# Kernel optimization log

Hardware: AMD Instinct MI355X
Metric: run time of the kernel (lower is better)

Reference implementation:

```python
import jax, jax.numpy as jnp
import numpy as np

D_MODEL = 1024
N_HEADS = 16
NUM_KV_HEADS = 4
D_K = D_MODEL // N_HEADS
ROPE_BASE = 10000.0


def apply_rotary_emb(x, base=ROPE_BASE):
    # x: [B, H, T, D], half-split rotation over positions 0..T-1
    B, H, T, D = x.shape
    inv_freq = 1.0 / (base ** (jnp.arange(0, D, 2, dtype=jnp.float32) / D))  # [D/2]
    ang = jnp.arange(T, dtype=jnp.float32)[:, None] * inv_freq[None, :]      # [T, D/2]
    cos = jnp.cos(ang)[None, None].astype(x.dtype)
    sin = jnp.sin(ang)[None, None].astype(x.dtype)
    x1, x2 = x[..., : D // 2], x[..., D // 2 :]
    return jnp.concatenate([x1 * cos - x2 * sin, x2 * cos + x1 * sin], axis=-1)


def setup_inputs() -> dict:
    key = jax.random.key(0)
    ks = jax.random.split(key, 6)
    B, Tq, Tkv = 4, 2048, 2048
    query = jax.random.normal(ks[0], (B, Tq, D_MODEL), dtype=jnp.float32)
    key_value = jax.random.normal(ks[1], (B, Tkv, D_MODEL), dtype=jnp.float32)
    query_mask = jnp.ones((B, Tq), dtype=jnp.bool_)
    kv_mask = jnp.ones((B, Tkv), dtype=jnp.bool_)
    s = 0.02
    w_q = jax.random.normal(ks[2], (D_MODEL, D_MODEL), dtype=jnp.float32) * s
    w_k = jax.random.normal(ks[3], (NUM_KV_HEADS * D_K, D_MODEL), dtype=jnp.float32) * s
    w_v = jax.random.normal(ks[4], (NUM_KV_HEADS * D_K, D_MODEL), dtype=jnp.float32) * s
    w_out = jax.random.normal(ks[5], (D_MODEL, D_MODEL), dtype=jnp.float32) * s
    return {"query": query, "key_value": key_value, "query_mask": query_mask,
            "kv_mask": kv_mask, "w_q": w_q, "w_k": w_k, "w_v": w_v, "w_out": w_out}


def reference(query, key_value, query_mask, kv_mask, w_q, w_k, w_v, w_out):
    B, Tq, _ = query.shape
    Tkv = key_value.shape[1]
    group = N_HEADS // NUM_KV_HEADS
    # projections (torch Linear: x @ W.T)
    Q = (query @ w_q.T).reshape(B, Tq, N_HEADS, D_K).transpose(0, 2, 1, 3)        # [B,H,Tq,D]
    K = (key_value @ w_k.T).reshape(B, Tkv, NUM_KV_HEADS, D_K).transpose(0, 2, 1, 3)
    V = (key_value @ w_v.T).reshape(B, Tkv, NUM_KV_HEADS, D_K).transpose(0, 2, 1, 3)
    # RoPE on Q and K
    Q = apply_rotary_emb(Q)
    K = apply_rotary_emb(K)
    # GQA: repeat kv heads
    K = jnp.repeat(K, group, axis=1)  # [B,H,Tkv,D]
    V = jnp.repeat(V, group, axis=1)
    # mask: [B,1,Tq,Tkv]
    attn_mask = (kv_mask[:, None, None, :] & query_mask[:, None, :, None])
    scale = 1.0 / jnp.sqrt(jnp.asarray(D_K, dtype=Q.dtype))
    scores = jnp.einsum("bhqd,bhkd->bhqk", Q, K) * scale
    scores = jnp.where(attn_mask, scores, jnp.asarray(-jnp.inf, dtype=scores.dtype))
    attn = jax.nn.softmax(scores, axis=-1)
    out = jnp.einsum("bhqk,bhkd->bhqd", attn, V)
    out = out.transpose(0, 2, 1, 3).reshape(B, Tq, D_MODEL)
    out = out @ w_out.T
    return out
```

## Files before the change

### kernel.cpp

```cpp
#include <hip/hip_runtime.h>
#include <hip/hip_bf16.h>
#include <hip/hip_fp16.h>

#define B_    4
#define TQ    2048
#define TKV   2048
#define DM    1024
#define NH    16
#define NKV   4
#define DK    64

typedef _Float16 f16x8 __attribute__((ext_vector_type(8)));
typedef _Float16 f16x4 __attribute__((ext_vector_type(4)));
typedef float    f32x4 __attribute__((ext_vector_type(4)));
typedef float    f32x16 __attribute__((ext_vector_type(16)));

__device__ __forceinline__ void store1(float* p, float v) { *p = v; }
__device__ __forceinline__ void store1(__half* p, float v) {
  union { __half h; unsigned short u; } c; c.h = __float2half(v);
  *(unsigned short*)p = c.u;
}

__device__ __forceinline__ f16x4 load4h(const float* p) {
  float4 v = *(const float4*)p;
  f16x4 r;
  r[0] = (_Float16)v.x; r[1] = (_Float16)v.y;
  r[2] = (_Float16)v.z; r[3] = (_Float16)v.w;
  return r;
}
__device__ __forceinline__ f16x4 load4h(const __half* p) {
  return *(const f16x4*)p;
}

__device__ __forceinline__ unsigned pack2h(float a, float b) {
  auto pk = __builtin_amdgcn_cvt_pkrtz(a, b);
  unsigned u;
  __builtin_memcpy(&u, &pk, 4);
  return u;
}

__global__ void zero_out_kernel(float* out, int n) {
  int i = blockIdx.x * blockDim.x + threadIdx.x;
  if (i < n) out[i] = 0.0f;
}

#define GAP 40
template <typename AT, typename CT>
__global__ __launch_bounds__(256) void gemm_bt_mfma(
    const AT* __restrict__ A,
    const float* __restrict__ W0, const float* __restrict__ W1,
    CT* __restrict__ C0, CT* __restrict__ C1, int M, int N, int K) {
  __shared__ _Float16 As[2 * 128 * GAP];
  __shared__ _Float16 Ws[2 * 128 * GAP];
  const float* __restrict__ W = (blockIdx.z == 0) ? W0 : W1;
  CT* __restrict__ C = (blockIdx.z == 0) ? C0 : C1;

  const int t = threadIdx.x;
  const int w = t >> 6, l = t & 63;
  const int lm = l & 15, quad = l >> 4;
  const int wm = (w >> 1) * 64, wn = (w & 1) * 64;
  const int m0 = blockIdx.y * 128, n0 = blockIdx.x * 128;

  const int srow = t >> 3;
  const int scol = (t & 7) * 4;

  f32x4 acc[4][4] = {};
  f16x4 av[4], wv[4];
#pragma unroll
  for (int p = 0; p < 4; ++p) {
    int r = srow + p * 32;
    av[p] = load4h(&A[(size_t)(m0 + r) * K + scol]);
    wv[p] = load4h(&W[(size_t)(n0 + r) * K + scol]);
  }

  int cur = 0;
  for (int k0 = 0; k0 < K; k0 += 32) {
    _Float16* as = &As[cur * 128 * GAP];
    _Float16* ws = &Ws[cur * 128 * GAP];
#pragma unroll
    for (int p = 0; p < 4; ++p) {
      int r = srow + p * 32;
      *(f16x4*)&as[r * GAP + scol] = av[p];
      *(f16x4*)&ws[r * GAP + scol] = wv[p];
    }
    __syncthreads();
    if (k0 + 32 < K) {
#pragma unroll
      for (int p = 0; p < 4; ++p) {
        int r = srow + p * 32;
        av[p] = load4h(&A[(size_t)(m0 + r) * K + k0 + 32 + scol]);
        wv[p] = load4h(&W[(size_t)(n0 + r) * K + k0 + 32 + scol]);
      }
    }

    f16x8 af[4], bf[4];
#pragma unroll
    for (int i = 0; i < 4; ++i)
      af[i] = *(const f16x8*)&as[(wm + i * 16 + lm) * GAP + quad * 8];
#pragma unroll
    for (int j = 0; j < 4; ++j)
      bf[j] = *(const f16x8*)&ws[(wn + j * 16 + lm) * GAP + quad * 8];
#pragma unroll
    for (int i = 0; i < 4; ++i)
#pragma unroll
      for (int j = 0; j < 4; ++j)
        acc[i][j] =
            __builtin_amdgcn_mfma_f32_16x16x32_f16(af[i], bf[j], acc[i][j], 0, 0, 0);
    cur ^= 1;
  }

#pragma unroll
  for (int i = 0; i < 4; ++i)
#pragma unroll
    for (int r = 0; r < 4; ++r) {
      size_t row = (size_t)(m0 + wm + i * 16 + quad * 4 + r) * N;
#pragma unroll
      for (int j = 0; j < 4; ++j)
        store1(&C[row + n0 + wn + j * 16 + lm], acc[i][j][r]);
    }
}

__global__ void rope_kernel(__half* __restrict__ X, int T, int H, int total_pairs) {
  int idx = blockIdx.x * blockDim.x + threadIdx.x;
  if (idx >= total_pairs) return;
  int i   = idx & 31;
  int h   = (idx >> 5) % H;
  int row = idx / (32 * H);
  int tpos = row % T;
  __half* p = X + ((size_t)row * H + h) * DK;
  float inv = exp2f((float)i * -0.41524101186091403f);
  float ang = (float)tpos * inv;
  float c, s;
  sincosf(ang, &s, &c);
  float x1 = __half2float(p[i]), x2 = __half2float(p[i + 32]);
  p[i]      = __float2half(x1 * c - x2 * s);
  p[i + 32] = __float2half(x2 * c + x1 * s);
}

#define AP 72
#define C2 0.18033688011112042f
#define RLOG2 -0.41524101186091403f
__global__ __launch_bounds__(256, 3) void attn_mfma(const __half* Q,
                                                    const __half* __restrict__ K,
                                                    const __half* __restrict__ V,
                                                    __half* O) {
  __shared__ _Float16 Ks[64 * AP];
  __shared__ _Float16 Vt[64 * AP];
  const int t = threadIdx.x;
  const int w = t >> 6, l = t & 63;
  const int lq = l & 31, hi = l >> 5;
  const int qt = blockIdx.x, h = blockIdx.y, b = blockIdx.z;
  const int kvh = h >> 2;

  const __half* qbase =
      Q + (((size_t)b * TQ + qt * 128 + w * 32 + lq) * NH + h) * DK;
  f16x8 aq[4];
#pragma unroll
  for (int kc = 0; kc < 4; ++kc)
    aq[kc] = *(const f16x8*)(qbase + kc * 16 + hi * 8);

  {
    const float tpos = (float)(qt * 128 + w * 32 + lq);
#pragma unroll
    for (int kc = 0; kc < 2; ++kc)
#pragma unroll
      for (int j = 0; j < 8; ++j) {
        int d = kc * 16 + hi * 8 + j;
        float inv = exp2f((float)d * RLOG2);
        float ang = tpos * inv;
        float c, s;
        sincosf(ang, &s, &c);
        float x1 = (float)aq[kc][j], x2 = (float)aq[kc + 2][j];
        aq[kc][j]     = (_Float16)((x1 * c - x2 * s) * C2);
        aq[kc + 2][j] = (_Float16)((x2 * c + x1 * s) * C2);
      }
  }

  const int skey = t >> 3, sdseg = t & 7;
  const int vkey = t & 63, vdb0 = (t >> 6) * 8;
  const __half* kp0 =
      K + (((size_t)b * TKV + skey) * NKV + kvh) * DK + sdseg * 8;
  const __half* kp1 = kp0 + (size_t)32 * NKV * DK;
  const __half* vp0 =
      V + (((size_t)b * TKV + vkey) * NKV + kvh) * DK + vdb0;
  const __half* vp1 = vp0 + 32;
  const size_t kstep = (size_t)64 * NKV * DK;

  f16x8 kpre0 = *(const f16x8*)kp0, kpre1 = *(const f16x8*)kp1;
  f16x8 vpre0 = *(const f16x8*)vp0, vpre1 = *(const f16x8*)vp1;

  f32x16 o_acc[2];
#pragma unroll
  for (int i = 0; i < 16; ++i) { o_acc[0][i] = 0.f; o_acc[1][i] = 0.f; }
  float m_run = -1e30f, l_run = 0.0f;

  for (int ck = 0; ck < TKV / 64; ++ck) {
    __syncthreads();
    *(f16x8*)&Ks[skey * AP + sdseg * 8] = kpre0;
    *(f16x8*)&Ks[(skey + 32) * AP + sdseg * 8] = kpre1;
#pragma unroll
    for (int j = 0; j < 8; ++j) {
      Vt[(vdb0 + j) * AP + vkey] = vpre0[j];
      Vt[(vdb0 + 32 + j) * AP + vkey] = vpre1[j];
    }
    __syncthreads();
    if (ck + 1 < TKV / 64) {
      size_t off = (size_t)(ck + 1) * kstep;
      kpre0 = *(const f16x8*)(kp0 + off);
      kpre1 = *(const f16x8*)(kp1 + off);
      vpre0 = *(const f16x8*)(vp0 + off);
      vpre1 = *(const f16x8*)(vp1 + off);
    }

#pragma unroll
    for (int tile = 0; tile < 2; ++tile) {
      f32x16 st;
#pragma unroll
      for (int i = 0; i < 16; ++i) st[i] = 0.f;
      __builtin_amdgcn_s_setprio(1);
#pragma unroll
      for (int kc = 0; kc < 4; ++kc) {
        f16x8 ak =
            *(const f16x8*)&Ks[(tile * 32 + lq) * AP + kc * 16 + hi * 8];
        st = __builtin_amdgcn_mfma_f32_32x32x16_f16(ak, aq[kc], st, 0, 0, 0);
      }
      __builtin_amdgcn_s_setprio(0);

      float vmax = st[0];
#pragma unroll
      for (int i = 1; i < 16; ++i) vmax = fmaxf(vmax, st[i]);
      vmax = fmaxf(vmax, __shfl_xor(vmax, 32));

      if (!__all(vmax - m_run <= 8.0f)) {
        float m_new = fmaxf(m_run, vmax);
        float alpha = exp2f(m_run - m_new);
        m_run = m_new;
        l_run *= alpha;
#pragma unroll
        for (int reg = 0; reg < 16; ++reg) {
          int row = (reg & 3) + 8 * (reg >> 2) + 4 * hi;
          float ar = __shfl(alpha, row);
          o_acc[0][reg] *= ar;
          o_acc[1][reg] *= ar;
        }
      }

      unsigned q16u[8];
      float psum = 0.0f;
#pragma unroll
      for (int rr = 0; rr < 8; ++rr) {
        float p0 = exp2f(st[2 * rr] - m_run);
        float p1 = exp2f(st[2 * rr + 1] - m_run);
        psum += p0 + p1;
        q16u[rr] = pack2h(p0, p1);
      }
      psum += __shfl_xor(psum, 32);
      l_run += psum;

      __builtin_amdgcn_s_setprio(1);
#pragma unroll
      for (int kb = 0; kb < 2; ++kb) {
        const int base = kb * 4;
        union { unsigned u[4]; f16x8 v; } ap;
#pragma unroll
        for (int c = 0; c < 2; ++c) {
          unsigned R0 = q16u[base + c];
          unsigned R1 = q16u[base + 2 + c];
          unsigned Z = hi ? R0 : R1;
          unsigned Xp = __shfl_xor(Z, 32);
          ap.u[c]     = hi ? Xp : R0;
          ap.u[c + 2] = hi ? R1 : Xp;
        }
#pragma unroll
        for (int nt = 0; nt < 2; ++nt) {
          f16x8 bv = *(const f16x8*)&Vt[(nt * 32 + lq) * AP + tile * 32 +
                                        kb * 16 + hi * 8];
          o_acc[nt] =
              __builtin_amdgcn_mfma_f32_32x32x16_f16(ap.v, bv, o_acc[nt], 0, 0, 0);
        }
      }
      __builtin_amdgcn_s_setprio(0);
    }
  }

#pragma unroll
  for (int reg = 0; reg < 16; ++reg) {
    int row = (reg & 3) + 8 * (reg >> 2) + 4 * hi;
    float inv = 1.0f / __shfl(l_run, row);
    size_t orow =
        (((size_t)b * TQ + qt * 128 + w * 32 + row) * NH + h) * DK;
    O[orow + lq]      = __float2half(o_acc[0][reg] * inv);
    O[orow + 32 + lq] = __float2half(o_acc[1][reg] * inv);
  }
}

extern "C" void kernel_launch(void* const* d_in, const int* in_sizes, int n_in,
                              void* d_out, int out_size, void* d_ws, size_t ws_size,
                              hipStream_t stream) {
  int iq, ikv, iwq, iwk, iwv, iwo;
  bool ok = true;
  if (n_in >= 8 && in_sizes[0] == 8388608 && in_sizes[1] == 8388608) {
    iq = 0; ikv = 1; iwq = 4; iwk = 5; iwv = 6; iwo = 7;
  } else if (n_in >= 8 && in_sizes[0] == 8388608 && in_sizes[1] == 8192) {
    ikv = 0; iq = 2; iwk = 4; iwo = 5; iwq = 6; iwv = 7;
  } else if (n_in == 6 && in_sizes[2] == 1048576) {
    iq = 0; ikv = 1; iwq = 2; iwk = 3; iwv = 4; iwo = 5;
  } else if (n_in == 6 && in_sizes[2] == 262144) {
    ikv = 0; iq = 1; iwk = 2; iwo = 3; iwq = 4; iwv = 5;
  } else {
    ok = false; iq = ikv = iwq = iwk = iwv = iwo = 0;
  }

  const size_t nQ  = (size_t)B_ * TQ * DM;
  const size_t nKV = (size_t)B_ * TKV * NKV * DK;
  const size_t need = (nQ + 2 * nKV) * sizeof(__half);
  if (!ok || ws_size < need) {
    zero_out_kernel<<<(out_size + 255) / 256, 256, 0, stream>>>((float*)d_out,
                                                                out_size);
    return;
  }

  const float* query     = (const float*)d_in[iq];
  const float* key_value = (const float*)d_in[ikv];
  const float* w_q   = (const float*)d_in[iwq];
  const float* w_k   = (const float*)d_in[iwk];
  const float* w_v   = (const float*)d_in[iwv];
  const float* w_out = (const float*)d_in[iwo];
  float* out = (float*)d_out;

  __half* Qh = (__half*)d_ws;
  __half* Kh = Qh + nQ;
  __half* Vh = Kh + nKV;

  dim3 blk(256);
  gemm_bt_mfma<<<dim3(DM / 128, B_ * TQ / 128, 1), blk, 0, stream>>>(
      query, w_q, w_q, Qh, Qh, B_ * TQ, DM, DM);
  gemm_bt_mfma<<<dim3(NKV * DK / 128, B_ * TKV / 128, 2), blk, 0, stream>>>(
      key_value, w_k, w_v, Kh, Vh, B_ * TKV, NKV * DK, DM);
  int pk = B_ * TKV * NKV * 32;
  rope_kernel<<<(pk + 255) / 256, blk, 0, stream>>>(Kh, TKV, NKV, pk);
  attn_mfma<<<dim3(TQ / 128, NH, B_), dim3(256), 0, stream>>>(Qh, Kh, Vh, Qh);
  gemm_bt_mfma<<<dim3(DM / 128, B_ * TQ / 128, 1), blk, 0, stream>>>(
      Qh, w_out, w_out, out, out, B_ * TQ, DM, DM);
}
```

Baseline: 387.8 us.

## Merge Q/K/V projections into one launch with 64x128 GEMM tiles

```diff
diff --git a/kernel.cpp b/kernel.cpp
--- a/kernel.cpp
+++ b/kernel.cpp
@@ -45,63 +45,80 @@
 }
 
 #define GAP 40
+#define BM 64
+#define BN 128
 template <typename AT, typename CT>
-__global__ __launch_bounds__(256) void gemm_bt_mfma(
-    const AT* __restrict__ A,
+__global__ __launch_bounds__(256) void gemm_proj(
+    const AT* __restrict__ A0, const AT* __restrict__ A1,
     const float* __restrict__ W0, const float* __restrict__ W1,
-    CT* __restrict__ C0, CT* __restrict__ C1, int M, int N, int K) {
-  __shared__ _Float16 As[2 * 128 * GAP];
-  __shared__ _Float16 Ws[2 * 128 * GAP];
-  const float* __restrict__ W = (blockIdx.z == 0) ? W0 : W1;
-  CT* __restrict__ C = (blockIdx.z == 0) ? C0 : C1;
+    const float* __restrict__ W2,
+    CT* __restrict__ C0, CT* __restrict__ C1, CT* __restrict__ C2,
+    int N0, int Nkv, int K) {
+  const int bid = blockIdx.x;
+  const AT* __restrict__ A;
+  const float* __restrict__ W;
+  CT* __restrict__ C;
+  int N, bx, by;
+  if (bid < 1024) {
+    A = A0; W = W0; C = C0; N = N0;
+    bx = bid & 7; by = bid >> 3;
+  } else {
+    int r = bid - 1024;
+    A = A1; N = Nkv;
+    if (r < 256) { W = W1; C = C1; } else { W = W2; C = C2; r -= 256; }
+    bx = r & 1; by = r >> 1;
+  }
+
+  __shared__ _Float16 As[2 * BM * GAP];
+  __shared__ _Float16 Ws[2 * BN * GAP];
 
   const int t = threadIdx.x;
   const int w = t >> 6, l = t & 63;
   const int lm = l & 15, quad = l >> 4;
-  const int wm = (w >> 1) * 64, wn = (w & 1) * 64;
-  const int m0 = blockIdx.y * 128, n0 = blockIdx.x * 128;
+  const int wm = (w >> 1) * 32, wn = (w & 1) * 64;
+  const int m0 = by * BM, n0 = bx * BN;
 
   const int srow = t >> 3;
   const int scol = (t & 7) * 4;
 
-  f32x4 acc[4][4] = {};
-  f16x4 av[4], wv[4];
-#pragma unroll
-  for (int p = 0; p < 4; ++p) {
-    int r = srow + p * 32;
-    av[p] = load4h(&A[(size_t)(m0 + r) * K + scol]);
-    wv[p] = load4h(&W[(size_t)(n0 + r) * K + scol]);
-  }
+  f32x4 acc[2][4] = {};
+  f16x4 av[2], wv[4];
+#pragma unroll
+  for (int p = 0; p < 2; ++p)
+    av[p] = load4h(&A[(size_t)(m0 + srow + p * 32) * K + scol]);
+#pragma unroll
+  for (int p = 0; p < 4; ++p)
+    wv[p] = load4h(&W[(size_t)(n0 + srow + p * 32) * K + scol]);
 
   int cur = 0;
   for (int k0 = 0; k0 < K; k0 += 32) {
-    _Float16* as = &As[cur * 128 * GAP];
-    _Float16* ws = &Ws[cur * 128 * GAP];
-#pragma unroll
-    for (int p = 0; p < 4; ++p) {
-      int r = srow + p * 32;
-      *(f16x4*)&as[r * GAP + scol] = av[p];
-      *(f16x4*)&ws[r * GAP + scol] = wv[p];
-    }
+    _Float16* as = &As[cur * BM * GAP];
+    _Float16* ws = &Ws[cur * BN * GAP];
+#pragma unroll
+    for (int p = 0; p < 2; ++p)
+      *(f16x4*)&as[(srow + p * 32) * GAP + scol] = av[p];
+#pragma unroll
+    for (int p = 0; p < 4; ++p)
+      *(f16x4*)&ws[(srow + p * 32) * GAP + scol] = wv[p];
     __syncthreads();
     if (k0 + 32 < K) {
 #pragma unroll
-      for (int p = 0; p < 4; ++p) {
-        int r = srow + p * 32;
-        av[p] = load4h(&A[(size_t)(m0 + r) * K + k0 + 32 + scol]);
-        wv[p] = load4h(&W[(size_t)(n0 + r) * K + k0 + 32 + scol]);
-      }
-    }
-
-    f16x8 af[4], bf[4];
-#pragma unroll
-    for (int i = 0; i < 4; ++i)
+      for (int p = 0; p < 2; ++p)
+        av[p] = load4h(&A[(size_t)(m0 + srow + p * 32) * K + k0 + 32 + scol]);
+#pragma unroll
+      for (int p = 0; p < 4; ++p)
+        wv[p] = load4h(&W[(size_t)(n0 + srow + p * 32) * K + k0 + 32 + scol]);
+    }
+
+    f16x8 af[2], bf[4];
+#pragma unroll
+    for (int i = 0; i < 2; ++i)
       af[i] = *(const f16x8*)&as[(wm + i * 16 + lm) * GAP + quad * 8];
 #pragma unroll
     for (int j = 0; j < 4; ++j)
       bf[j] = *(const f16x8*)&ws[(wn + j * 16 + lm) * GAP + quad * 8];
 #pragma unroll
-    for (int i = 0; i < 4; ++i)
+    for (int i = 0; i < 2; ++i)
 #pragma unroll
       for (int j = 0; j < 4; ++j)
         acc[i][j] =
@@ -110,7 +127,7 @@
   }
 
 #pragma unroll
-  for (int i = 0; i < 4; ++i)
+  for (int i = 0; i < 2; ++i)
 #pragma unroll
     for (int r = 0; r < 4; ++r) {
       size_t row = (size_t)(m0 + wm + i * 16 + quad * 4 + r) * N;
@@ -333,13 +350,11 @@
   __half* Vh = Kh + nKV;
 
   dim3 blk(256);
-  gemm_bt_mfma<<<dim3(DM / 128, B_ * TQ / 128, 1), blk, 0, stream>>>(
-      query, w_q, w_q, Qh, Qh, B_ * TQ, DM, DM);
-  gemm_bt_mfma<<<dim3(NKV * DK / 128, B_ * TKV / 128, 2), blk, 0, stream>>>(
-      key_value, w_k, w_v, Kh, Vh, B_ * TKV, NKV * DK, DM);
+  gemm_proj<<<dim3(1536), blk, 0, stream>>>(query, key_value, w_q, w_k, w_v,
+                                            Qh, Kh, Vh, DM, NKV * DK, DM);
   int pk = B_ * TKV * NKV * 32;
   rope_kernel<<<(pk + 255) / 256, blk, 0, stream>>>(Kh, TKV, NKV, pk);
   attn_mfma<<<dim3(TQ / 128, NH, B_), dim3(256), 0, stream>>>(Qh, Kh, Vh, Qh);
-  gemm_bt_mfma<<<dim3(DM / 128, B_ * TQ / 128, 1), blk, 0, stream>>>(
-      Qh, w_out, w_out, out, out, B_ * TQ, DM, DM);
-}
+  gemm_proj<<<dim3(1024), blk, 0, stream>>>(Qh, Qh, w_out, w_out, w_out,
+                                            out, out, out, DM, DM, DM);
+}
```

Measured after the change: 363.8 us. 1.07x faster.
